# Kernel optimization log

Measured on AMD Instinct MI355X. Metric: run time of the kernel, lower is better.

Reference implementation:

```python
import jax, jax.numpy as jnp
import numpy as np

A, B, OBS, ACT, H, G = 8, 4096, 512, 64, 1024, 64
N, E = 10000, 40000
NODE, GH, NTYPES, AEMB = 32, 64, 8, 16


def _ln(x, g, b, eps=1e-5):
    m = jnp.mean(x, -1, keepdims=True)
    v = jnp.mean((x - m) ** 2, -1, keepdims=True)
    return (x - m) * jax.lax.rsqrt(v + eps) * g + b


def _neigh_mean(h, edges, n):
    # undirected mean aggregation: each dependency edge contributes both ways
    s, d = edges[:, 0], edges[:, 1]
    agg = jnp.zeros((n, h.shape[-1]), h.dtype).at[d].add(h[s]).at[s].add(h[d])
    deg = jnp.zeros((n,), h.dtype).at[d].add(1.0).at[s].add(1.0)
    return agg / jnp.maximum(deg, 1.0)[:, None]


def setup_inputs() -> dict:
    key = jax.random.key(0)
    ks = jax.random.split(key, 32)
    f32 = jnp.float32

    def w(k, i, o):
        return (jax.random.normal(k, (i, o), f32) / np.sqrt(i)).astype(f32)

    d = {}
    d["observations"] = jax.random.normal(ks[0], (A, B, OBS), f32)
    d["node_types"] = jax.random.randint(ks[1], (N,), 0, NTYPES)
    d["node_agents"] = jax.random.randint(ks[2], (N,), 0, A)
    d["edges"] = jax.random.randint(ks[3], (E, 2), 0, N)
    # graph encoder params
    d["type_embed"] = (jax.random.normal(ks[4], (NTYPES, NODE), f32) * 0.02).astype(f32)
    d["gagent_embed"] = (jax.random.normal(ks[5], (A, NODE), f32) * 0.02).astype(f32)
    d["W_l0"] = w(ks[6], 2 * NODE, GH); d["b_l0"] = jnp.zeros((GH,), f32)
    d["g_l0"] = jnp.ones((GH,), f32);   d["be_l0"] = jnp.zeros((GH,), f32)
    d["W_l1"] = w(ks[7], GH + GH, G);   d["b_l1"] = jnp.zeros((G,), f32)
    d["g_l1"] = jnp.ones((G,), f32);    d["be_l1"] = jnp.zeros((G,), f32)
    d["W_gp"] = w(ks[8], G, G);         d["b_gp"] = jnp.zeros((G,), f32)
    # shared policy params
    d["agent_embed"] = (jax.random.normal(ks[9], (A, AEMB), f32) * 0.02).astype(f32)
    d["Wp1"] = w(ks[10], OBS + G + AEMB, H); d["bp1"] = jnp.zeros((H,), f32)
    d["Wp2"] = w(ks[11], H, H);              d["bp2"] = jnp.zeros((H,), f32)
    d["Wp3"] = w(ks[12], H, ACT);            d["bp3"] = jnp.zeros((ACT,), f32)
    # value head params
    d["Wv1"] = w(ks[13], OBS * A + G, H); d["bv1"] = jnp.zeros((H,), f32)
    d["Wv2"] = w(ks[14], H, H);           d["bv2"] = jnp.zeros((H,), f32)
    d["Wv3"] = w(ks[15], H, 1);           d["bv3"] = jnp.zeros((1,), f32)
    return d


def _forward(observations, node_types, node_agents, edges,
             type_embed, gagent_embed, W_l0, b_l0, g_l0, be_l0,
             W_l1, b_l1, g_l1, be_l1, W_gp, b_gp,
             agent_embed, Wp1, bp1, Wp2, bp2, Wp3, bp3,
             Wv1, bv1, Wv2, bv2, Wv3, bv3):
    # --- graph encoder ---
    x = jnp.concatenate([type_embed[node_types], gagent_embed[node_agents]], -1)  # [N,64]
    # layer 0: aggregation is computed-but-ignored in the original; combined = x
    h = _ln(jax.nn.relu(x @ W_l0 + b_l0), g_l0, be_l0)                 # [N,GH]
    agg = _neigh_mean(h, edges, N)                                     # [N,GH]
    h = _ln(jax.nn.relu(jnp.concatenate([h, agg], -1) @ W_l1 + b_l1), g_l1, be_l1)  # [N,G]
    graph_embed = jnp.mean(h, 0) @ W_gp + b_gp                         # [G]

    ge = jnp.broadcast_to(graph_embed, (B, G))                         # [B,G]
    # --- shared policy over agents ---
    ae = jnp.broadcast_to(agent_embed[:, None, :], (A, B, AEMB))
    geA = jnp.broadcast_to(graph_embed, (A, B, G))
    comb = jnp.concatenate([observations, geA, ae], -1)                # [A,B,OBS+G+16]
    hp = jax.nn.relu(jnp.einsum("abi,io->abo", comb, Wp1) + bp1)
    hp = jax.nn.relu(jnp.einsum("abi,io->abo", hp, Wp2) + bp2)
    logits = jnp.einsum("abi,io->abo", hp, Wp3) + bp3                  # [A,B,ACT]
    # --- value head ---
    joint = jnp.transpose(observations, (1, 0, 2)).reshape(B, A * OBS)
    vin = jnp.concatenate([joint, ge], -1)                             # [B, A*OBS+G]
    hv = jax.nn.relu(vin @ Wv1 + bv1)
    hv = jax.nn.relu(hv @ Wv2 + bv2)
    value = hv @ Wv3 + bv3                                             # [B,1]
    return logits, value


def reference(observations, node_types, node_agents, edges,
              type_embed, gagent_embed, W_l0, b_l0, g_l0, be_l0,
              W_l1, b_l1, g_l1, be_l1, W_gp, b_gp,
              agent_embed, Wp1, bp1, Wp2, bp2, Wp3, bp3,
              Wv1, bv1, Wv2, bv2, Wv3, bv3):
    return _forward(observations, node_types, node_agents, edges,
                    type_embed, gagent_embed, W_l0, b_l0, g_l0, be_l0,
                    W_l1, b_l1, g_l1, be_l1, W_gp, b_gp,
                    agent_embed, Wp1, bp1, Wp2, bp2, Wp3, bp3,
                    Wv1, bv1, Wv2, bv2, Wv3, bv3)
```

## Files before the change

kernel.cpp:

```cpp
#include <hip/hip_runtime.h>
#include <hip/hip_bf16.h>

#define A_ 8
#define B_ 4096
#define OBS_ 512
#define ACT_ 64
#define H_ 1024
#define G_ 64
#define N_ 10000
#define E_ 40000

using bf16 = __hip_bfloat16;
typedef __attribute__((ext_vector_type(8))) short short8;
typedef __attribute__((ext_vector_type(4))) float f32x4;

__device__ __forceinline__ float wsum(float v) {
#pragma unroll
  for (int off = 32; off >= 1; off >>= 1) v += __shfl_xor(v, off, 64);
  return v;
}

__device__ __forceinline__ void storeC(float* p, float v) { *p = v; }
__device__ __forceinline__ void storeC(bf16* p, float v) { *p = __float2bfloat16(v); }

__device__ __forceinline__ unsigned short f2bu(float x) {
  bf16 h = __float2bfloat16(x);
  unsigned short u;
  __builtin_memcpy(&u, &h, 2);
  return u;
}

__device__ __forceinline__ void gload_lds16(const bf16* g, const void* lds_uniform) {
  __builtin_amdgcn_global_load_lds(
      (const __attribute__((address_space(1))) unsigned int*)g,
      (__attribute__((address_space(3))) unsigned int*)lds_uniform, 16, 0, 0);
}

template <int N>
__device__ __forceinline__ void waitvm() {
#define WV_CASE(n) if constexpr (N == n) asm volatile("s_waitcnt vmcnt(" #n ")" ::: "memory");
  WV_CASE(0) WV_CASE(1) WV_CASE(2) WV_CASE(3) WV_CASE(4) WV_CASE(5) WV_CASE(6) WV_CASE(7)
  WV_CASE(8) WV_CASE(9) WV_CASE(10) WV_CASE(12) WV_CASE(16)
  static_assert(N <= 16, "vmcnt too large");
#undef WV_CASE
}

__global__ __launch_bounds__(256) void prep_k(
    const float* __restrict__ obs, bf16* __restrict__ joint,
    const float* __restrict__ Wp1, bf16* __restrict__ Wp1t,
    const float* __restrict__ Wp2, bf16* __restrict__ Wp2t,
    const float* __restrict__ Wp3, bf16* __restrict__ Wp3t,
    const float* __restrict__ Wv1, bf16* __restrict__ Wv1t,
    const float* __restrict__ Wv2, bf16* __restrict__ Wv2t,
    const int* __restrict__ node_types, const int* __restrict__ node_agents,
    const float* __restrict__ type_embed, const float* __restrict__ gagent_embed,
    const float* __restrict__ W_l0, const float* __restrict__ b_l0,
    const float* __restrict__ g_l0, const float* __restrict__ be_l0,
    float* __restrict__ h0, float* __restrict__ agg, float* __restrict__ deg) {
  __shared__ float shb[32 * 33];
  const int bid = blockIdx.x, tid = threadIdx.x;
  if (bid < 8192) {
    size_t i = ((size_t)bid * 256 + tid) * 8;
    int a = (int)(i >> 21);
    int rem = (int)(i & ((1u << 21) - 1));
    int b = rem >> 9, k = rem & 511;
    const float* p = obs + i;
    short8 o;
#pragma unroll
    for (int t = 0; t < 8; t++) o[t] = (short)f2bu(p[t]);
    *(short8*)(joint + (size_t)b * 4096 + a * 512 + k) = o;
  } else if (bid < 14912) {
    int b = bid - 8192;
    const float* W;
    bf16* Wt;
    int K, N;
    if (b < 512) { W = Wp1; Wt = Wp1t; K = 512; N = 1024; }
    else if (b < 1536) { W = Wp2; Wt = Wp2t; K = 1024; N = 1024; b -= 512; }
    else if (b < 1600) { W = Wp3; Wt = Wp3t; K = 1024; N = 64; b -= 1536; }
    else if (b < 5696) { W = Wv1; Wt = Wv1t; K = 4096; N = 1024; b -= 1600; }
    else { W = Wv2; Wt = Wv2t; K = 1024; N = 1024; b -= 5696; }
    int nx = N >> 5;
    int n0 = (b % nx) * 32, k0 = (b / nx) * 32;
    int tx = tid & 31, ty = tid >> 5;
    float(*t2)[33] = (float(*)[33])shb;
#pragma unroll
    for (int r = ty; r < 32; r += 8) t2[r][tx] = W[(size_t)(k0 + r) * N + n0 + tx];
    __syncthreads();
#pragma unroll
    for (int r = ty; r < 32; r += 8)
      Wt[(size_t)(n0 + r) * K + k0 + tx] = __float2bfloat16(t2[tx][r]);
  } else {
    int nb = bid - 14912;
    int w = tid >> 6, t = tid & 63;
    int n = nb * 4 + w;
    float* xx = shb + w * 64;
    int ty2 = node_types[n], ag = node_agents[n];
    xx[t] = (t < 32) ? type_embed[ty2 * 32 + t] : gagent_embed[ag * 32 + (t - 32)];
    agg[(size_t)n * 64 + t] = 0.f;
    if (t == 0) deg[n] = 0.f;
    __syncthreads();
    float acc = b_l0[t];
#pragma unroll 8
    for (int i = 0; i < 64; i++) acc += xx[i] * W_l0[i * 64 + t];
    acc = fmaxf(acc, 0.f);
    float m = wsum(acc) * (1.f / 64.f);
    float d = acc - m;
    float v = wsum(d * d) * (1.f / 64.f);
    h0[(size_t)n * 64 + t] = d * rsqrtf(v + 1e-5f) * g_l0[t] + be_l0[t];
  }
}

__global__ void edge_k(const int* __restrict__ edges, const float* __restrict__ h0,
                       float* __restrict__ agg, float* __restrict__ deg) {
  int idx = blockIdx.x * 256 + threadIdx.x;
  if (idx >= E_ * 64) return;
  int e = idx >> 6, c = idx & 63;
  int s = edges[e * 2 + 0], d = edges[e * 2 + 1];
  atomicAdd(&agg[(size_t)d * 64 + c], h0[(size_t)s * 64 + c]);
  atomicAdd(&agg[(size_t)s * 64 + c], h0[(size_t)d * 64 + c]);
  if (c == 0) { atomicAdd(&deg[d], 1.f); atomicAdd(&deg[s], 1.f); }
}

__global__ __launch_bounds__(256) void gnn_l1_k(
    const float* __restrict__ h0, const float* __restrict__ agg, const float* __restrict__ deg,
    const float* __restrict__ W, const float* __restrict__ b, const float* __restrict__ g,
    const float* __restrict__ be, float* __restrict__ h1) {
  __shared__ float x[4][128];
  int w = threadIdx.x >> 6, t = threadIdx.x & 63;
  int n = blockIdx.x * 4 + w;
  x[w][t] = h0[(size_t)n * 64 + t];
  x[w][64 + t] = agg[(size_t)n * 64 + t] / fmaxf(deg[n], 1.0f);
  __syncthreads();
  float acc = b[t];
#pragma unroll 8
  for (int i = 0; i < 128; i++) acc += x[w][i] * W[i * 64 + t];
  acc = fmaxf(acc, 0.f);
  float m = wsum(acc) * (1.f / 64.f);
  float d = acc - m;
  float v = wsum(d * d) * (1.f / 64.f);
  h1[(size_t)n * 64 + t] = d * rsqrtf(v + 1e-5f) * g[t] + be[t];
}

__global__ void colmean_k(const float* __restrict__ h1, float* __restrict__ meanv) {
  int c = blockIdx.x, t = threadIdx.x;
  float s = 0.f;
  for (int n = t; n < N_; n += 256) s += h1[(size_t)n * 64 + c];
  __shared__ float red[256];
  red[t] = s;
  __syncthreads();
  for (int off = 128; off >= 1; off >>= 1) {
    if (t < off) red[t] += red[t + off];
    __syncthreads();
  }
  if (t == 0) meanv[c] = red[0] / (float)N_;
}

__global__ void fused_bias_k(const float* __restrict__ meanv, const float* __restrict__ Wgp,
                             const float* __restrict__ bgp, const float* __restrict__ agent_embed,
                             const float* __restrict__ Wp1, const float* __restrict__ bp1,
                             const float* __restrict__ Wv1, const float* __restrict__ bv1,
                             const float* __restrict__ bv3,
                             float* __restrict__ biasA, float* __restrict__ biasV,
                             float* __restrict__ value) {
  __shared__ float ge[64];
  int t = threadIdx.x;
  int gidx = blockIdx.x * 256 + t;
  if (gidx < B_) value[gidx] = bv3[0];
  if (t < 64) {
    float s = bgp[t];
    for (int g2 = 0; g2 < 64; g2++) s += meanv[g2] * Wgp[g2 * 64 + t];
    ge[t] = s;
  }
  __syncthreads();
  int blk = blockIdx.x;
  if (blk < 32) {
    int idx = blk * 256 + t;
    int a = idx >> 10, o = idx & 1023;
    float s = bp1[o];
    for (int g2 = 0; g2 < 64; g2++) s += ge[g2] * Wp1[(size_t)(512 + g2) * 1024 + o];
    for (int e = 0; e < 16; e++) s += agent_embed[a * 16 + e] * Wp1[(size_t)(576 + e) * 1024 + o];
    biasA[idx] = s;
  } else {
    int o = (blk - 32) * 256 + t;
    float s = bv1[o];
    for (int g2 = 0; g2 < 64; g2++) s += ge[g2] * Wv1[(size_t)(4096 + g2) * 1024 + o];
    biasV[o] = s;
  }
}

#define BARR()                        \
  asm volatile("" ::: "memory");      \
  __builtin_amdgcn_s_barrier();       \
  asm volatile("" ::: "memory")

#define RD8(off) (*(const short8*)(sb + (off)))

#define MMQ(FI0)                                                                     \
  __builtin_amdgcn_s_setprio(1);                                                     \
  acc[FI0 + 0][0] = __builtin_amdgcn_mfma_f32_16x16x32_bf16(a0, b0, acc[FI0 + 0][0], 0, 0, 0); \
  acc[FI0 + 0][1] = __builtin_amdgcn_mfma_f32_16x16x32_bf16(a0, b1, acc[FI0 + 0][1], 0, 0, 0); \
  acc[FI0 + 0][2] = __builtin_amdgcn_mfma_f32_16x16x32_bf16(a0, b2, acc[FI0 + 0][2], 0, 0, 0); \
  acc[FI0 + 0][3] = __builtin_amdgcn_mfma_f32_16x16x32_bf16(a0, b3, acc[FI0 + 0][3], 0, 0, 0); \
  acc[FI0 + 1][0] = __builtin_amdgcn_mfma_f32_16x16x32_bf16(a1, b0, acc[FI0 + 1][0], 0, 0, 0); \
  acc[FI0 + 1][1] = __builtin_amdgcn_mfma_f32_16x16x32_bf16(a1, b1, acc[FI0 + 1][1], 0, 0, 0); \
  acc[FI0 + 1][2] = __builtin_amdgcn_mfma_f32_16x16x32_bf16(a1, b2, acc[FI0 + 1][2], 0, 0, 0); \
  acc[FI0 + 1][3] = __builtin_amdgcn_mfma_f32_16x16x32_bf16(a1, b3, acc[FI0 + 1][3], 0, 0, 0); \
  acc[FI0 + 2][0] = __builtin_amdgcn_mfma_f32_16x16x32_bf16(a2, b0, acc[FI0 + 2][0], 0, 0, 0); \
  acc[FI0 + 2][1] = __builtin_amdgcn_mfma_f32_16x16x32_bf16(a2, b1, acc[FI0 + 2][1], 0, 0, 0); \
  acc[FI0 + 2][2] = __builtin_amdgcn_mfma_f32_16x16x32_bf16(a2, b2, acc[FI0 + 2][2], 0, 0, 0); \
  acc[FI0 + 2][3] = __builtin_amdgcn_mfma_f32_16x16x32_bf16(a2, b3, acc[FI0 + 2][3], 0, 0, 0); \
  acc[FI0 + 3][0] = __builtin_amdgcn_mfma_f32_16x16x32_bf16(a3, b0, acc[FI0 + 3][0], 0, 0, 0); \
  acc[FI0 + 3][1] = __builtin_amdgcn_mfma_f32_16x16x32_bf16(a3, b1, acc[FI0 + 3][1], 0, 0, 0); \
  acc[FI0 + 3][2] = __builtin_amdgcn_mfma_f32_16x16x32_bf16(a3, b2, acc[FI0 + 3][2], 0, 0, 0); \
  acc[FI0 + 3][3] = __builtin_amdgcn_mfma_f32_16x16x32_bf16(a3, b3, acc[FI0 + 3][3], 0, 0, 0); \
  __builtin_amdgcn_s_setprio(0)

template <int AMODE, int BIASMODE, bool RELU, typename TC>
__launch_bounds__(512, 1)
__global__ void g11_k(const bf16* __restrict__ Ap, const bf16* __restrict__ Bt,
                      const float* __restrict__ biasp, TC* __restrict__ Cp,
                      int M, int N, int K) {
  constexpr int SBUF = 65536;
  __shared__ char smem[2 * SBUF];

  const int tid = threadIdx.x;
  const int wid = tid >> 6, lane = tid & 63;
  const int wm = wid >> 2, wn = wid & 3;
  const int l15 = lane & 15;

  const int nwg = gridDim.x * gridDim.y;
  int fid = blockIdx.y * gridDim.x + blockIdx.x;
  int swz = (fid & 7) * (nwg >> 3) + (fid >> 3);
  const int m0 = (swz / gridDim.x) * 256;
  const int n0 = (swz % gridDim.x) * 256;

  f32x4 acc[8][4];
#pragma unroll
  for (int i = 0; i < 8; i++)
#pragma unroll
    for (int j = 0; j < 4; j++) acc[i][j] = (f32x4){0.f, 0.f, 0.f, 0.f};

  const bf16* pg[8];
  {
    int srow = tid >> 3;
    int c = (tid & 7) ^ (srow & 7);
#pragma unroll
    for (int g = 0; g < 4; ++g) {
      int r = m0 + g * 64 + srow;
      if (AMODE == 0)
        pg[g] = Ap + (size_t)r * K + c * 8;
      else
        pg[g] = Ap + (((size_t)(r & (B_ - 1))) << 12) + ((size_t)(r >> 12) << 9) + c * 8;
    }
#pragma unroll
    for (int g = 4; g < 8; ++g) {
      int r = n0 + (g - 4) * 64 + srow;
      pg[g] = Bt + (size_t)r * K + c * 8;
    }
  }

  const int slot0 = (lane >> 4) ^ (l15 & 7);
  const int aof0 = (wm * 128 + l15) * 128 + slot0 * 16;
  const int bof0 = 32768 + (wn * 64 + l15) * 128 + slot0 * 16;
  const int aof1 = aof0 ^ 64;
  const int bof1 = bof0 ^ 64;

#define STG(g, buf)                                                    \
  {                                                                    \
    gload_lds16(pg[g], smem + (buf) * SBUF + (g) * 8192 + wid * 1024); \
    pg[g] += 64;                                                       \
  }

  STG(0, 0) STG(2, 0) STG(4, 0) STG(5, 0) STG(6, 0) STG(7, 0) STG(1, 0) STG(3, 0)
  waitvm<0>();
  BARR();

  const int nt = K >> 6;
  for (int t = 0; t < nt; ++t) {
    const int cb = t & 1, ob = cb ^ 1;
    const bool last = (t == nt - 1);
    const char* sb = smem + cb * SBUF;
    short8 a0, a1, a2, a3, b0, b1, b2, b3;
    a0 = RD8(aof0 + 0 * 2048); a1 = RD8(aof0 + 1 * 2048);
    a2 = RD8(aof0 + 2 * 2048); a3 = RD8(aof0 + 3 * 2048);
    b0 = RD8(bof0 + 0 * 2048); b1 = RD8(bof0 + 1 * 2048);
    b2 = RD8(bof0 + 2 * 2048); b3 = RD8(bof0 + 3 * 2048);
    if (!last) { STG(0, ob) STG(2, ob) }
    BARR();
    MMQ(0);
    if (last) waitvm<0>(); else waitvm<2>();
    BARR();
    a0 = RD8(aof0 + 4 * 2048); a1 = RD8(aof0 + 5 * 2048);
    a2 = RD8(aof0 + 6 * 2048); a3 = RD8(aof0 + 7 * 2048);
    if (!last) { STG(4, ob) STG(5, ob) }
    BARR();
    MMQ(4);
    BARR();
    a0 = RD8(aof1 + 0 * 2048); a1 = RD8(aof1 + 1 * 2048);
    a2 = RD8(aof1 + 2 * 2048); a3 = RD8(aof1 + 3 * 2048);
    b0 = RD8(bof1 + 0 * 2048); b1 = RD8(bof1 + 1 * 2048);
    b2 = RD8(bof1 + 2 * 2048); b3 = RD8(bof1 + 3 * 2048);
    if (!last) { STG(6, ob) STG(7, ob) }
    BARR();
    MMQ(0);
    BARR();
    a0 = RD8(aof1 + 4 * 2048); a1 = RD8(aof1 + 5 * 2048);
    a2 = RD8(aof1 + 6 * 2048); a3 = RD8(aof1 + 7 * 2048);
    if (!last) { STG(1, ob) STG(3, ob) }
    BARR();
    MMQ(4);
    if (!last) waitvm<2>(); else waitvm<0>();
    BARR();
  }
#undef STG

#pragma unroll
  for (int i = 0; i < 8; ++i) {
    int rb = m0 + wm * 128 + i * 16 + (lane >> 4) * 4;
#pragma unroll
    for (int j = 0; j < 4; ++j) {
      int col = n0 + wn * 64 + j * 16 + l15;
#pragma unroll
      for (int r = 0; r < 4; r++) {
        int row = rb + r;
        float bias = (BIASMODE == 0) ? biasp[col] : biasp[((row >> 12) << 10) + col];
        float v = acc[i][j][r] + bias;
        if (RELU) v = fmaxf(v, 0.f);
        storeC(&Cp[(size_t)row * N + col], v);
      }
    }
  }
}

template <int FM, int FN, int WAVES_M, int WAVES_N, int DEPTH, int AMODE, int BIASMODE, bool RELU,
          typename TC, int VOUT = 0>
__launch_bounds__(WAVES_M * WAVES_N * 64, 2)
__global__ void pgemm_k(const bf16* __restrict__ Ap, const bf16* __restrict__ Bt,
                        const float* __restrict__ biasp, TC* __restrict__ Cp,
                        int M, int N, int K,
                        const float* __restrict__ Wv3 = nullptr,
                        float* __restrict__ vout = nullptr) {
  constexpr int NTHR = WAVES_M * WAVES_N * 64;
  constexpr int AR = WAVES_M * FM * 16;
  constexpr int BR = WAVES_N * FN * 16;
  constexpr int RPG = NTHR / 4;
  constexpr int AG = AR / RPG;
  constexpr int BG = BR / RPG;
  constexpr int G = AG + BG;
  constexpr int GRP = NTHR * 16;
  constexpr int ABYTES = AR * 64;
  constexpr int SBUF = (AR + BR) * 64;
  constexpr int NB = DEPTH + 1;
  __shared__ char smem[NB * SBUF];

  const int tid = threadIdx.x;
  const int wid = tid >> 6, lane = tid & 63;
  const int wm = wid / WAVES_N, wn = wid % WAVES_N;
  const int l15 = lane & 15;

  const int nwg = gridDim.x * gridDim.y;
  int fid = blockIdx.y * gridDim.x + blockIdx.x;
  int swz = (fid & 7) * (nwg >> 3) + (fid >> 3);
  const int m0 = (swz / gridDim.x) * AR;
  const int n0 = (swz % gridDim.x) * BR;

  f32x4 acc[FM][FN];
#pragma unroll
  for (int i = 0; i < FM; i++)
#pragma unroll
    for (int j = 0; j < FN; j++) acc[i][j] = (f32x4){0.f, 0.f, 0.f, 0.f};

  const bf16* pa[AG];
  const bf16* pb[BG];
  {
    int row = tid >> 2;
    int c = (tid & 3) ^ ((tid >> 3) & 3);
#pragma unroll
    for (int q = 0; q < AG; ++q) {
      int r = m0 + q * RPG + row;
      if (AMODE == 0)
        pa[q] = Ap + (size_t)r * K + c * 8;
      else
        pa[q] = Ap + (((size_t)(r & (B_ - 1))) << 12) + ((size_t)(r >> 12) << 9) + c * 8;
    }
#pragma unroll
    for (int q = 0; q < BG; ++q) {
      int r = n0 + q * RPG + row;
      pb[q] = Bt + (size_t)r * K + c * 8;
    }
  }

  const int cA = (lane >> 4) ^ ((l15 >> 1) & 3);
  const int offA0 = (wm * FM * 16 + l15) * 64 + cA * 16;
  const int offB0 = ABYTES + (wn * FN * 16 + l15) * 64 + cA * 16;

  auto stage = [&](int buf) {
    char* base = smem + buf * SBUF;
#pragma unroll
    for (int q = 0; q < AG; ++q) {
      gload_lds16(pa[q], base + q * GRP + wid * 1024);
      pa[q] += 32;
    }
#pragma unroll
    for (int q = 0; q < BG; ++q) {
      gload_lds16(pb[q], base + ABYTES + q * GRP + wid * 1024);
      pb[q] += 32;
    }
  };

  auto comp = [&](int buf) {
    const char* sb = smem + buf * SBUF;
    short8 bfr[FN];
#pragma unroll
    for (int j = 0; j < FN; ++j) bfr[j] = *(const short8*)(sb + offB0 + j * 1024);
    constexpr int FH = (FM > 4) ? FM / 2 : FM;
#pragma unroll
    for (int h = 0; h < FM / FH; ++h) {
      short8 afr[FH];
#pragma unroll
      for (int i = 0; i < FH; ++i) afr[i] = *(const short8*)(sb + offA0 + (h * FH + i) * 1024);
      __builtin_amdgcn_s_setprio(1);
#pragma unroll
      for (int i = 0; i < FH; ++i)
#pragma unroll
        for (int j = 0; j < FN; ++j)
          acc[h * FH + i][j] =
              __builtin_amdgcn_mfma_f32_16x16x32_bf16(afr[i], bfr[j], acc[h * FH + i][j], 0, 0, 0);
      __builtin_amdgcn_s_setprio(0);
    }
  };

  const int nt = K >> 5;
#pragma unroll
  for (int q = 0; q < DEPTH; ++q) stage(q);
  int cbuf = 0, sbi = DEPTH;
  for (int T = 0; T < nt - DEPTH; ++T) {
    stage(sbi);
    if (++sbi == NB) sbi = 0;
    waitvm<DEPTH * G>();
    __builtin_amdgcn_s_barrier();
    asm volatile("" ::: "memory");
    comp(cbuf);
    if (++cbuf == NB) cbuf = 0;
    asm volatile("" ::: "memory");
    __builtin_amdgcn_s_barrier();
  }
#define DRAIN(d)                       \
  {                                    \
    waitvm<(d) * G>();                 \
    __builtin_amdgcn_s_barrier();      \
    asm volatile("" ::: "memory");     \
    comp(cbuf);                        \
    if (++cbuf == NB) cbuf = 0;        \
    asm volatile("" ::: "memory");     \
  }
  if constexpr (DEPTH == 4) { DRAIN(3) DRAIN(2) }
  DRAIN(1)
  DRAIN(0)
#undef DRAIN

#pragma unroll
  for (int i = 0; i < FM; ++i) {
    int rb = m0 + wm * FM * 16 + i * 16 + (lane >> 4) * 4;
    if constexpr (VOUT) {
#pragma unroll
      for (int r = 0; r < 4; r++) {
        int row = rb + r;
        float s = 0.f;
#pragma unroll
        for (int j = 0; j < FN; ++j) {
          int col = n0 + wn * FN * 16 + j * 16 + l15;
          float v = acc[i][j][r] + biasp[col];
          if (RELU) v = fmaxf(v, 0.f);
          s += v * Wv3[col];
        }
        s += __shfl_xor(s, 1, 64);
        s += __shfl_xor(s, 2, 64);
        s += __shfl_xor(s, 4, 64);
        s += __shfl_xor(s, 8, 64);
        if (l15 == 0) atomicAdd(&vout[row], s);
      }
    } else {
#pragma unroll
      for (int j = 0; j < FN; ++j) {
        int col = n0 + wn * FN * 16 + j * 16 + l15;
#pragma unroll
        for (int r = 0; r < 4; r++) {
          int row = rb + r;
          float bias = (BIASMODE == 0) ? biasp[col] : biasp[((row >> 12) << 10) + col];
          float v = acc[i][j][r] + bias;
          if (RELU) v = fmaxf(v, 0.f);
          storeC(&Cp[(size_t)row * N + col], v);
        }
      }
    }
  }
}

extern "C" void kernel_launch(void* const* d_in, const int* in_sizes, int n_in,
                              void* d_out, int out_size, void* d_ws, size_t ws_size,
                              hipStream_t stream) {
  const float* obs = (const float*)d_in[0];
  const int* node_types = (const int*)d_in[1];
  const int* node_agents = (const int*)d_in[2];
  const int* edges = (const int*)d_in[3];
  const float* type_embed = (const float*)d_in[4];
  const float* gagent_embed = (const float*)d_in[5];
  const float* W_l0 = (const float*)d_in[6];
  const float* b_l0 = (const float*)d_in[7];
  const float* g_l0 = (const float*)d_in[8];
  const float* be_l0 = (const float*)d_in[9];
  const float* W_l1 = (const float*)d_in[10];
  const float* b_l1 = (const float*)d_in[11];
  const float* g_l1 = (const float*)d_in[12];
  const float* be_l1 = (const float*)d_in[13];
  const float* W_gp = (const float*)d_in[14];
  const float* b_gp = (const float*)d_in[15];
  const float* agent_embed = (const float*)d_in[16];
  const float* Wp1 = (const float*)d_in[17];
  const float* bp1 = (const float*)d_in[18];
  const float* Wp2 = (const float*)d_in[19];
  const float* bp2 = (const float*)d_in[20];
  const float* Wp3 = (const float*)d_in[21];
  const float* bp3 = (const float*)d_in[22];
  const float* Wv1 = (const float*)d_in[23];
  const float* bv1 = (const float*)d_in[24];
  const float* Wv2 = (const float*)d_in[25];
  const float* bv2 = (const float*)d_in[26];
  const float* Wv3 = (const float*)d_in[27];
  const float* bv3 = (const float*)d_in[28];

  char* wsp = (char*)d_ws;
  auto alloc = [&](size_t bytes) {
    char* p = wsp;
    wsp += (bytes + 255) & ~(size_t)255;
    return p;
  };
  float* h0 = (float*)alloc((size_t)N_ * 64 * 4);
  float* agg = (float*)alloc((size_t)N_ * 64 * 4);
  float* deg = (float*)alloc((size_t)N_ * 4);
  float* h1 = (float*)alloc((size_t)N_ * 64 * 4);
  float* meanv = (float*)alloc(64 * 4);
  float* biasA = (float*)alloc(8 * 1024 * 4);
  float* biasV = (float*)alloc(1024 * 4);
  bf16* joint = (bf16*)alloc((size_t)4096 * 4096 * 2);
  bf16* Wp1t = (bf16*)alloc((size_t)1024 * 512 * 2);
  bf16* Wp2t = (bf16*)alloc((size_t)1024 * 1024 * 2);
  bf16* Wp3t = (bf16*)alloc((size_t)64 * 1024 * 2);
  bf16* Wv1t = (bf16*)alloc((size_t)1024 * 4096 * 2);
  bf16* Wv2t = (bf16*)alloc((size_t)1024 * 1024 * 2);
  bf16* C1 = (bf16*)alloc((size_t)32768 * 1024 * 2);
  bf16* C2 = (bf16*)alloc((size_t)32768 * 1024 * 2);
  bf16* hv = (bf16*)alloc((size_t)4096 * 1024 * 2);

  float* logits = (float*)d_out;
  float* value = (float*)d_out + (size_t)A_ * B_ * ACT_;

  prep_k<<<17412, 256, 0, stream>>>(obs, joint, Wp1, Wp1t, Wp2, Wp2t, Wp3, Wp3t, Wv1, Wv1t, Wv2,
                                    Wv2t, node_types, node_agents, type_embed, gagent_embed, W_l0,
                                    b_l0, g_l0, be_l0, h0, agg, deg);
  edge_k<<<(E_ * 64) / 256, 256, 0, stream>>>(edges, h0, agg, deg);
  gnn_l1_k<<<N_ / 4, 256, 0, stream>>>(h0, agg, deg, W_l1, b_l1, g_l1, be_l1, h1);
  colmean_k<<<64, 256, 0, stream>>>(h1, meanv);
  fused_bias_k<<<36, 256, 0, stream>>>(meanv, W_gp, b_gp, agent_embed, Wp1, bp1, Wv1, bv1, bv3,
                                       biasA, biasV, value);

  g11_k<1, 1, true, bf16>
      <<<dim3(4, 128), 512, 0, stream>>>(joint, Wp1t, biasA, C1, 32768, 1024, 512);
  g11_k<0, 0, true, bf16>
      <<<dim3(4, 128), 512, 0, stream>>>(C1, Wp2t, bp2, C2, 32768, 1024, 1024);
  pgemm_k<4, 2, 2, 2, 2, 0, 0, false, float>
      <<<dim3(1, 256), 256, 0, stream>>>(C2, Wp3t, bp3, logits, 32768, 64, 1024);
  pgemm_k<4, 4, 2, 2, 2, 0, 0, true, bf16>
      <<<dim3(8, 32), 256, 0, stream>>>(joint, Wv1t, biasV, hv, 4096, 1024, 4096);
  pgemm_k<4, 4, 2, 2, 2, 0, 0, true, bf16, 1>
      <<<dim3(8, 32), 256, 0, stream>>>(hv, Wv2t, bv2, (bf16*)nullptr, 4096, 1024, 1024, Wv3,
                                        value);
}
```

Before: 280.0 us.

## Switch big GEMM to 4-stage K=32 LDS pipeline with 3 tiles in flight

The 256x256 MFMA GEMM kernel used for the two large policy layers now splits K into 32-wide tiles held in four 32KB LDS buffers, instead of 64-wide tiles in two 64KB buffers. Global-to-LDS loads run three tiles ahead, with a new XOR swizzle suited to 64-byte rows. The wait counts are adjusted for the pipeline tail. The aim is to hide global load latency better. The cost is twice as many loop iterations and barriers per unit of K, and more complex vmcnt accounting.

New measurement: 286.0 us. 1.02x slower.

```diff
diff --git a/kernel.cpp b/kernel.cpp
--- a/kernel.cpp
+++ b/kernel.cpp
@@ -217,11 +217,11 @@
 
 template <int AMODE, int BIASMODE, bool RELU, typename TC>
 __launch_bounds__(512, 1)
-__global__ void g11_k(const bf16* __restrict__ Ap, const bf16* __restrict__ Bt,
+__global__ void g12_k(const bf16* __restrict__ Ap, const bf16* __restrict__ Bt,
                       const float* __restrict__ biasp, TC* __restrict__ Cp,
                       int M, int N, int K) {
-  constexpr int SBUF = 65536;
-  __shared__ char smem[2 * SBUF];
+  constexpr int TBUF = 32768;
+  __shared__ char smem[4 * TBUF];
 
   const int tid = threadIdx.x;
   const int wid = tid >> 6, lane = tid & 63;
@@ -240,76 +240,64 @@
 #pragma unroll
     for (int j = 0; j < 4; j++) acc[i][j] = (f32x4){0.f, 0.f, 0.f, 0.f};
 
-  const bf16* pg[8];
+  const bf16* pg[4];
   {
-    int srow = tid >> 3;
-    int c = (tid & 7) ^ (srow & 7);
-#pragma unroll
-    for (int g = 0; g < 4; ++g) {
-      int r = m0 + g * 64 + srow;
-      if (AMODE == 0)
-        pg[g] = Ap + (size_t)r * K + c * 8;
-      else
-        pg[g] = Ap + (((size_t)(r & (B_ - 1))) << 12) + ((size_t)(r >> 12) << 9) + c * 8;
-    }
-#pragma unroll
-    for (int g = 4; g < 8; ++g) {
-      int r = n0 + (g - 4) * 64 + srow;
-      pg[g] = Bt + (size_t)r * K + c * 8;
-    }
-  }
-
-  const int slot0 = (lane >> 4) ^ (l15 & 7);
-  const int aof0 = (wm * 128 + l15) * 128 + slot0 * 16;
-  const int bof0 = 32768 + (wn * 64 + l15) * 128 + slot0 * 16;
-  const int aof1 = aof0 ^ 64;
-  const int bof1 = bof0 ^ 64;
+    int srow = tid >> 2;
+    int c = (tid & 3) ^ ((srow >> 1) & 3);
+    int rA0 = m0 + srow, rA1 = m0 + 128 + srow;
+    if (AMODE == 0) {
+      pg[0] = Ap + (size_t)rA0 * K + c * 8;
+      pg[1] = Ap + (size_t)rA1 * K + c * 8;
+    } else {
+      pg[0] = Ap + (((size_t)(rA0 & (B_ - 1))) << 12) + ((size_t)(rA0 >> 12) << 9) + c * 8;
+      pg[1] = Ap + (((size_t)(rA1 & (B_ - 1))) << 12) + ((size_t)(rA1 >> 12) << 9) + c * 8;
+    }
+    pg[2] = Bt + (size_t)(n0 + srow) * K + c * 8;
+    pg[3] = Bt + (size_t)(n0 + 128 + srow) * K + c * 8;
+  }
+
+  const int rA = wm * 128 + l15;
+  const int offA = rA * 64 + (((lane >> 4) ^ ((rA >> 1) & 3))) * 16;
+  const int rB = wn * 64 + l15;
+  const int offB = 16384 + rB * 64 + (((lane >> 4) ^ ((rB >> 1) & 3))) * 16;
 
 #define STG(g, buf)                                                    \
   {                                                                    \
-    gload_lds16(pg[g], smem + (buf) * SBUF + (g) * 8192 + wid * 1024); \
-    pg[g] += 64;                                                       \
-  }
-
-  STG(0, 0) STG(2, 0) STG(4, 0) STG(5, 0) STG(6, 0) STG(7, 0) STG(1, 0) STG(3, 0)
-  waitvm<0>();
+    gload_lds16(pg[g], smem + (buf) * TBUF + (g) * 8192 + wid * 1024); \
+    pg[g] += 32;                                                       \
+  }
+
+#pragma unroll
+  for (int q = 0; q < 3; ++q) { STG(0, q) STG(1, q) STG(2, q) STG(3, q) }
+  waitvm<8>();
   BARR();
 
-  const int nt = K >> 6;
+  const int nt = K >> 5;
   for (int t = 0; t < nt; ++t) {
-    const int cb = t & 1, ob = cb ^ 1;
-    const bool last = (t == nt - 1);
-    const char* sb = smem + cb * SBUF;
+    const char* sb = smem + (t & 3) * TBUF;
+    const int ob = (t + 3) & 3;
+    const bool stg = (t + 3) < nt;
     short8 a0, a1, a2, a3, b0, b1, b2, b3;
-    a0 = RD8(aof0 + 0 * 2048); a1 = RD8(aof0 + 1 * 2048);
-    a2 = RD8(aof0 + 2 * 2048); a3 = RD8(aof0 + 3 * 2048);
-    b0 = RD8(bof0 + 0 * 2048); b1 = RD8(bof0 + 1 * 2048);
-    b2 = RD8(bof0 + 2 * 2048); b3 = RD8(bof0 + 3 * 2048);
-    if (!last) { STG(0, ob) STG(2, ob) }
-    BARR();
-    MMQ(0);
-    if (last) waitvm<0>(); else waitvm<2>();
-    BARR();
-    a0 = RD8(aof0 + 4 * 2048); a1 = RD8(aof0 + 5 * 2048);
-    a2 = RD8(aof0 + 6 * 2048); a3 = RD8(aof0 + 7 * 2048);
-    if (!last) { STG(4, ob) STG(5, ob) }
-    BARR();
-    MMQ(4);
-    BARR();
-    a0 = RD8(aof1 + 0 * 2048); a1 = RD8(aof1 + 1 * 2048);
-    a2 = RD8(aof1 + 2 * 2048); a3 = RD8(aof1 + 3 * 2048);
-    b0 = RD8(bof1 + 0 * 2048); b1 = RD8(bof1 + 1 * 2048);
-    b2 = RD8(bof1 + 2 * 2048); b3 = RD8(bof1 + 3 * 2048);
-    if (!last) { STG(6, ob) STG(7, ob) }
+    a0 = RD8(offA + 0 * 1024); a1 = RD8(offA + 1 * 1024);
+    a2 = RD8(offA + 2 * 1024); a3 = RD8(offA + 3 * 1024);
+    b0 = RD8(offB + 0 * 1024); b1 = RD8(offB + 1 * 1024);
+    b2 = RD8(offB + 2 * 1024); b3 = RD8(offB + 3 * 1024);
+    if (stg) { STG(0, ob) STG(1, ob) }
     BARR();
     MMQ(0);
     BARR();
-    a0 = RD8(aof1 + 4 * 2048); a1 = RD8(aof1 + 5 * 2048);
-    a2 = RD8(aof1 + 6 * 2048); a3 = RD8(aof1 + 7 * 2048);
-    if (!last) { STG(1, ob) STG(3, ob) }
+    a0 = RD8(offA + 4 * 1024); a1 = RD8(offA + 5 * 1024);
+    a2 = RD8(offA + 6 * 1024); a3 = RD8(offA + 7 * 1024);
+    if (stg) { STG(2, ob) STG(3, ob) }
     BARR();
     MMQ(4);
-    if (!last) waitvm<2>(); else waitvm<0>();
+    if (t + 4 <= nt) {
+      waitvm<8>();
+    } else if (t + 3 == nt) {
+      waitvm<4>();
+    } else if (t + 2 == nt) {
+      waitvm<0>();
+    }
     BARR();
   }
 #undef STG
@@ -565,9 +553,9 @@
   fused_bias_k<<<36, 256, 0, stream>>>(meanv, W_gp, b_gp, agent_embed, Wp1, bp1, Wv1, bv1, bv3,
                                        biasA, biasV, value);
 
-  g11_k<1, 1, true, bf16>
+  g12_k<1, 1, true, bf16>
       <<<dim3(4, 128), 512, 0, stream>>>(joint, Wp1t, biasA, C1, 32768, 1024, 512);
-  g11_k<0, 0, true, bf16>
+  g12_k<0, 0, true, bf16>
       <<<dim3(4, 128), 512, 0, stream>>>(C1, Wp2t, bp2, C2, 32768, 1024, 1024);
   pgemm_k<4, 2, 2, 2, 2, 0, 0, false, float>
       <<<dim3(1, 256), 256, 0, stream>>>(C2, Wp3t, bp3, logits, 32768, 64, 1024);
```
